# Kernel tuning notes

Hardware: AMD Instinct MI355X
Metric: run time of the kernel (lower is better)

## Reference

```python
import jax, jax.numpy as jnp
import numpy as np

# Dimensions pinned by the module: RelPosEmb1DAISummer(tokens=50, dim_head=124)
H = 8          # num_heads
D = 31         # channels // num_heads
T = 4          # time axis of the (p, t) spatial grid; D*T == 124 == dim_head
P = 50         # tokens
C = H * D      # 248 channels
SCALE = D ** -0.5  # note: module scales by d**-0.5 (=31), not (d*t)**-0.5 -- faithful


def rel_to_abs(x):
    """AI-Summer 1D relative->absolute reindexing. x: [b, h, l, 2l-1] -> [b, h, l, l]."""
    b, h, l, _ = x.shape
    x = jnp.pad(x, ((0, 0), (0, 0), (0, 0), (0, 1)))          # [b,h,l,2l]
    x = x.reshape(b, h, l * 2 * l)
    x = jnp.pad(x, ((0, 0), (0, 0), (0, l - 1)))
    x = x.reshape(b, h, l + 1, 2 * l - 1)
    return x[:, :, :l, l - 1:]


def setup_inputs() -> dict:
    key = jax.random.key(0)
    k1, k2, k3, k4 = jax.random.split(key, 4)
    B = 512
    x = jax.random.normal(k1, (B, C, P, T), jnp.float32)
    # 1x1 conv == per-position linear over channels: weight [3C, C], bias [3C]
    w_qkv = jax.random.normal(k2, (3 * C, C), jnp.float32) * (C ** -0.5)
    b_qkv = jax.random.normal(k3, (3 * C,), jnp.float32) * 0.01
    # shared-heads relative position embedding: [2*tokens-1, dim_head]
    rel_emb = jax.random.normal(k4, (2 * P - 1, D * T), jnp.float32) * ((D * T) ** -0.5)
    return {"x": x, "w_qkv": w_qkv, "b_qkv": b_qkv, "rel_emb": rel_emb}


def reference(x, w_qkv, b_qkv, rel_emb):
    B = x.shape[0]
    # 1x1 Conv2d: [B, C, P, T] -> [B, 3C, P, T]
    qkv = jnp.einsum('bcpt,oc->bopt', x, w_qkv) + b_qkv[None, :, None, None]
    # 'b (qkv h d) p t -> qkv b h d p t'
    qkv = qkv.reshape(B, 3, H, D, P, T)
    q, k, v = qkv[:, 0], qkv[:, 1], qkv[:, 2]                 # each [B,H,D,P,T]
    q = q.transpose(0, 1, 3, 2, 4).reshape(B, H, P, D * T)    # 'b h d p t -> b h p (d t)'
    k = k.transpose(0, 1, 2, 4, 3).reshape(B, H, D * T, P)    # 'b h d p t -> b h (d t) p'
    v = v.transpose(0, 1, 3, 2, 4).reshape(B, H, P, D * T)
    dots = jnp.einsum('bhpi,bhiq->bhpq', q, k)                # [B,H,P,P]
    bias = rel_to_abs(jnp.einsum('bhpd,rd->bhpr', q, rel_emb))
    attn = jax.nn.softmax((dots + bias) * SCALE, axis=-1)     # dropout = identity (eval)
    out = jnp.einsum('bhpq,bhqi->bhpi', attn, v)              # [B,H,P,D*T]
    # 'b h p (d t) -> b (h d) p t'
    out = out.reshape(B, H, P, D, T).transpose(0, 1, 3, 2, 4).reshape(B, H * D, P, T)
    return out
```

## Files before the change

### kernel.cpp

```cpp
#include <hip/hip_runtime.h>
#include <hip/hip_bf16.h>

typedef __bf16 bf16_t;
typedef bf16_t bf16x8 __attribute__((ext_vector_type(8)));
typedef bf16_t bf16x4 __attribute__((ext_vector_type(4)));
typedef float f32x4 __attribute__((ext_vector_type(4)));

constexpr float SCALE = 0.17960530202677491f;

__device__ __forceinline__ f32x4 mfma16(bf16x8 a, bf16x8 b, f32x4 c) {
    return __builtin_amdgcn_mfma_f32_16x16x32_bf16(a, b, c, 0, 0, 0);
}

__device__ __forceinline__ void opaque(bf16x8& v) {
    asm volatile("" : "+v"(v));
}

__global__ void prep_kernel(const float* __restrict__ w, const float* __restrict__ b_qkv,
                            const float* __restrict__ rel,
                            bf16_t* __restrict__ Wf, bf16_t* __restrict__ relf,
                            float* __restrict__ bp)
{
    int i = blockIdx.x * 256 + threadIdx.x;
    if (i < 196608) {
        int e = i & 7, lane = (i >> 3) & 63;
        int f = i >> 9;
        int ks = f & 7, g = f >> 3;
        int h = g / 6, m = g - h * 6;
        int r15 = lane & 15, g4 = lane >> 4;
        int s = m >> 1, d = ((m & 1) << 4) + r15;
        int c = ks * 32 + g4 * 8 + e;
        float v = 0.f;
        if (d < 31 && c < 248) v = w[(long)(s * 248 + h * 31 + d) * 248 + c];
        Wf[i] = (bf16_t)v;
        return;
    }
    i -= 196608;
    if (i < 14336) {
        int e = i & 7, lane = (i >> 3) & 63;
        int f = i >> 9;
        int ks = f & 3, rt = f >> 2;
        int r = rt * 16 + (lane & 15);
        int dt = ks * 32 + (lane >> 4) * 8 + e;
        float v = 0.f;
        if (r < 99 && dt < 124) v = rel[r * 124 + dt];
        relf[i] = (bf16_t)v;
        return;
    }
    i -= 14336;
    if (i < 768) {
        int h = i / 96, row = i - h * 96;
        int s = row >> 5, d = row & 31;
        bp[i] = (d < 31) ? b_qkv[s * 248 + h * 31 + d] : 0.f;
    }
}

__global__ void __launch_bounds__(512, 4)
fused_kernel(const float* __restrict__ x, const bf16_t* __restrict__ Wf,
             const bf16_t* __restrict__ relf, const float* __restrict__ bp,
             float* __restrict__ out)
{
    __shared__ __align__(16) bf16_t QH[64][128];
    __shared__ __align__(16) bf16_t KH[64][128];
    __shared__ __align__(16) bf16_t AS[64][64];
    __shared__ __align__(16) bf16_t VT[128][64];
    __shared__ float LS[50][68];

    const int b    = blockIdx.x;
    const int tid  = threadIdx.x;
    const int lane = tid & 63;
    const int w    = tid >> 6;
    const int r15  = lane & 15, g4 = lane >> 4;

    {
        *(f32x4*)((char*)&VT[0][0] + tid * 32)      = f32x4{0.f, 0.f, 0.f, 0.f};
        *(f32x4*)((char*)&VT[0][0] + tid * 32 + 16) = f32x4{0.f, 0.f, 0.f, 0.f};
        if (tid < 128) {
            int row = tid & 63;
            char* base = (tid < 64) ? (char*)&QH[0][0] : (char*)&KH[0][0];
            int chunk = 15 ^ (row & 7);
            *(long*)(base + row * 256 + chunk * 16 + 8) = 0L;
        }
    }

    const float* xb = x + (long)b * 49600;
    const int tile0 = w, tile1 = w + 8;
    const bool t1ok = (tile1 * 16 < 200);
    bf16x8 Areg[2][8];
#pragma unroll
    for (int ui = 0; ui < 2; ++ui) {
        int n = (w + 8 * ui) * 16 + r15;
        const float* xn = xb + n;
        bool nok = (n < 200);
#pragma unroll
        for (int ks = 0; ks < 8; ++ks) {
            bf16x8 fr;
#pragma unroll
            for (int e = 0; e < 8; ++e) {
                int c = ks * 32 + g4 * 8 + e;
                float v = (nok && c < 248) ? xn[(long)c * 200] : 0.f;
                fr[e] = (bf16_t)v;
            }
            Areg[ui][ks] = fr;
        }
    }
#pragma unroll
    for (int ui = 0; ui < 2; ++ui)
#pragma unroll
        for (int ks = 0; ks < 8; ++ks)
            opaque(Areg[ui][ks]);
    __syncthreads();

    const int qt  = w >> 1, par = w & 1;
    for (int h = 0; h < 8; ++h) {
        const bf16_t* wf = Wf + ((long)(h * 48) << 9) + lane * 8;
#pragma unroll
        for (int m = 0; m < 6; ++m) {
            f32x4 acc0 = f32x4{0.f, 0.f, 0.f, 0.f};
            f32x4 acc1 = f32x4{0.f, 0.f, 0.f, 0.f};
#pragma unroll
            for (int half = 0; half < 2; ++half) {
                bf16x8 Bc[4];
#pragma unroll
                for (int k4 = 0; k4 < 4; ++k4)
                    Bc[k4] = *(const bf16x8*)(wf + ((m * 8 + half * 4 + k4) << 9));
#pragma unroll
                for (int k4 = 0; k4 < 4; ++k4) {
                    int ks = half * 4 + k4;
                    acc0 = mfma16(Areg[0][ks], Bc[k4], acc0);
                    if (t1ok) acc1 = mfma16(Areg[1][ks], Bc[k4], acc1);
                }
            }
            int s = m >> 1;
            int d = ((m & 1) << 4) + r15;
            float bias = bp[h * 96 + m * 16 + r15];
            if (d < 31) {
#pragma unroll
                for (int ui = 0; ui < 2; ++ui) {
                    if (ui == 1 && !t1ok) continue;
                    f32x4 a = ui ? acc1 : acc0;
                    int p = (w + 8 * ui) * 4 + g4;
                    if (p >= 50) continue;
                    float a0 = a[0] + bias, a1 = a[1] + bias;
                    float a2 = a[2] + bias, a3 = a[3] + bias;
                    if (s < 2) {
                        bf16x4 pk = {(bf16_t)a0, (bf16_t)a1, (bf16_t)a2, (bf16_t)a3};
                        char* base = (s == 0) ? (char*)&QH[0][0] : (char*)&KH[0][0];
                        int chunk = (d >> 1) ^ (p & 7);
                        *(bf16x4*)(base + p * 256 + chunk * 16 + ((d & 1) << 3)) = pk;
                    } else {
                        int chunk = ((p >> 3) ^ (d & 7)) << 4;
                        char* vbase = (char*)&VT[0][0] + (d * 4) * 128 + chunk + (p & 7) * 2;
                        *(bf16_t*)(vbase)       = (bf16_t)a0;
                        *(bf16_t*)(vbase + 128) = (bf16_t)a1;
                        *(bf16_t*)(vbase + 256) = (bf16_t)a2;
                        *(bf16_t*)(vbase + 384) = (bf16_t)a3;
                    }
                }
            }
        }
        __syncthreads();

        bf16x8 Afr[4];
        {
            int p = qt * 16 + r15;
            int hp = p & 7;
#pragma unroll
            for (int ks = 0; ks < 4; ++ks)
                Afr[ks] = *(const bf16x8*)((char*)&QH[0][0] + p * 256 + ((((ks << 2) | g4) ^ hp) << 4));
        }
#pragma unroll
        for (int i = 0; i < 2; ++i) {
            int ct = par * 2 + i;
            int c = ct * 16 + r15;
            int hc = c & 7;
            f32x4 s = f32x4{0.f, 0.f, 0.f, 0.f};
#pragma unroll
            for (int ks = 0; ks < 4; ++ks) {
                bf16x8 Bf = *(const bf16x8*)((char*)&KH[0][0] + c * 256 + ((((ks << 2) | g4) ^ hc) << 4));
                s = mfma16(Afr[ks], Bf, s);
            }
            if (c < 50) {
#pragma unroll
                for (int j = 0; j < 4; ++j) {
                    int qrow = qt * 16 + g4 * 4 + j;
                    if (qrow < 50) LS[qrow][c] = s[j];
                }
            }
        }
        __syncthreads();

        {
            const bf16_t* rf = relf + lane * 8;
            for (int rt = par; rt < 7; rt += 2) {
                f32x4 s = f32x4{0.f, 0.f, 0.f, 0.f};
#pragma unroll
                for (int ks = 0; ks < 4; ++ks) {
                    bf16x8 R = *(const bf16x8*)(rf + ((rt * 4 + ks) << 9));
                    s = mfma16(Afr[ks], R, s);
                }
                int r = rt * 16 + r15;
#pragma unroll
                for (int j = 0; j < 4; ++j) {
                    int qrow = qt * 16 + g4 * 4 + j;
                    int jj = r + qrow - 49;
                    if (qrow < 50 && jj >= 0 && jj < 50) LS[qrow][jj] += s[j];
                }
            }
        }
        __syncthreads();

        {
            int row = tid >> 3, sub = tid & 7;
            int hrow = row & 7;
            if (row < 50) {
                float mx = -1e30f;
                for (int jj = sub; jj < 50; jj += 8) mx = fmaxf(mx, LS[row][jj]);
                mx = fmaxf(mx, __shfl_xor(mx, 1));
                mx = fmaxf(mx, __shfl_xor(mx, 2));
                mx = fmaxf(mx, __shfl_xor(mx, 4));
                float sum = 0.f;
                for (int jj = sub; jj < 50; jj += 8) {
                    float e = __expf((LS[row][jj] - mx) * SCALE);
                    LS[row][jj] = e;
                    sum += e;
                }
                sum += __shfl_xor(sum, 1);
                sum += __shfl_xor(sum, 2);
                sum += __shfl_xor(sum, 4);
                float rs = 1.f / sum;
                for (int jj = sub; jj < 64; jj += 8) {
                    float v = (jj < 50) ? LS[row][jj] * rs : 0.f;
                    *(bf16_t*)((char*)&AS[0][0] + row * 128 + (((jj >> 3) ^ hrow) << 4) + (jj & 7) * 2) = (bf16_t)v;
                }
            } else {
                for (int jj = sub; jj < 64; jj += 8)
                    *(bf16_t*)((char*)&AS[0][0] + row * 128 + (((jj >> 3) ^ hrow) << 4) + (jj & 7) * 2) = (bf16_t)0.f;
            }
        }
        __syncthreads();

        {
            int irow = w * 16 + r15;
            int hv = (irow >> 2) & 7;
            bf16x8 Av[2];
#pragma unroll
            for (int ks = 0; ks < 2; ++ks)
                Av[ks] = *(const bf16x8*)((char*)&VT[0][0] + irow * 128 + ((((ks << 2) | g4) ^ hv) << 4));
            int dd = w * 4 + g4;
#pragma unroll
            for (int pt = 0; pt < 4; ++pt) {
                int prow = pt * 16 + r15;
                int hp2 = prow & 7;
                f32x4 po = f32x4{0.f, 0.f, 0.f, 0.f};
#pragma unroll
                for (int ks = 0; ks < 2; ++ks) {
                    bf16x8 Bs = *(const bf16x8*)((char*)&AS[0][0] + prow * 128 + ((((ks << 2) | g4) ^ hp2) << 4));
                    po = mfma16(Av[ks], Bs, po);
                }
                if (dd < 31 && prow < 50)
                    *(f32x4*)(out + ((long)b * 248 + h * 31 + dd) * 200 + prow * 4) = po;
            }
        }
        __syncthreads();
    }
}

extern "C" void kernel_launch(void* const* d_in, const int* in_sizes, int n_in,
                              void* d_out, int out_size, void* d_ws, size_t ws_size,
                              hipStream_t stream)
{
    const float* x   = (const float*)d_in[0];
    const float* wq  = (const float*)d_in[1];
    const float* bq  = (const float*)d_in[2];
    const float* rel = (const float*)d_in[3];
    float* out = (float*)d_out;

    char* ws = (char*)d_ws;
    bf16_t* Wf   = (bf16_t*)ws;
    bf16_t* relf = (bf16_t*)(ws + 393216);
    float*  bp   = (float*)(ws + 421888);

    const int B = in_sizes[0] / 49600;

    prep_kernel<<<dim3(828), dim3(256), 0, stream>>>(wq, bq, rel, Wf, relf, bp);
    fused_kernel<<<dim3(B), dim3(512), 0, stream>>>(x, Wf, relf, bp, out);
}
```

Before: 205.4 us.

## Software-pipeline heads: split warps into score/softmax and PV groups with double buffers

Restructures the per-head loop into a two-stage pipeline. Warps 0-3 compute QK scores, the relative-position bias and the softmax for the current head. Warps 4-7 compute the attention-times-V output for the previous head, reading from double-buffered VT and AS regions carved out of one shared-memory array. This cuts the per-head barrier count from five to two, replacing intra-group barriers with lgkmcnt waits. It also prefetches weight and rel-embedding fragments one step ahead and folds SCALE into Q. The cost is more shared memory (about 80KB), which may lower occupancy, and an imbalanced split of work between the two warp groups.

New measurement: 346.2 us. +68.6%, slower.

```diff
diff --git a/kernel.cpp b/kernel.cpp
--- a/kernel.cpp
+++ b/kernel.cpp
@@ -8,10 +8,19 @@
 
 constexpr float SCALE = 0.17960530202677491f;
 
+#define QH_OFF 0
+#define KH_OFF 12800
+#define AS_OFF 25600
+#define VT_OFF 38400
+#define LS_OFF 70144
+#define SMEM_TOTAL 80544
+
 __device__ __forceinline__ f32x4 mfma16(bf16x8 a, bf16x8 b, f32x4 c) {
     return __builtin_amdgcn_mfma_f32_16x16x32_bf16(a, b, c, 0, 0, 0);
 }
-
+__device__ __forceinline__ void fence() {
+    asm volatile("s_waitcnt lgkmcnt(0)" ::: "memory");
+}
 __device__ __forceinline__ void opaque(bf16x8& v) {
     asm volatile("" : "+v"(v));
 }
@@ -60,12 +69,7 @@
              const bf16_t* __restrict__ relf, const float* __restrict__ bp,
              float* __restrict__ out)
 {
-    __shared__ __align__(16) bf16_t QH[64][128];
-    __shared__ __align__(16) bf16_t KH[64][128];
-    __shared__ __align__(16) bf16_t AS[64][64];
-    __shared__ __align__(16) bf16_t VT[128][64];
-    __shared__ float LS[50][68];
-
+    __shared__ __align__(16) char smem[SMEM_TOTAL];
     const int b    = blockIdx.x;
     const int tid  = threadIdx.x;
     const int lane = tid & 63;
@@ -73,19 +77,22 @@
     const int r15  = lane & 15, g4 = lane >> 4;
 
     {
-        *(f32x4*)((char*)&VT[0][0] + tid * 32)      = f32x4{0.f, 0.f, 0.f, 0.f};
-        *(f32x4*)((char*)&VT[0][0] + tid * 32 + 16) = f32x4{0.f, 0.f, 0.f, 0.f};
-        if (tid < 128) {
-            int row = tid & 63;
-            char* base = (tid < 64) ? (char*)&QH[0][0] : (char*)&KH[0][0];
+        f32x4 z = f32x4{0.f, 0.f, 0.f, 0.f};
+#pragma unroll
+        for (int k4 = 0; k4 < 4; ++k4) {
+            int idx = tid + k4 * 512;
+            if (idx < 1984) *(f32x4*)(smem + VT_OFF + idx * 16) = z;
+        }
+        if (tid < 100) {
+            int row = tid >> 1;
+            char* base = smem + ((tid & 1) ? KH_OFF : QH_OFF);
             int chunk = 15 ^ (row & 7);
             *(long*)(base + row * 256 + chunk * 16 + 8) = 0L;
         }
     }
 
     const float* xb = x + (long)b * 49600;
-    const int tile0 = w, tile1 = w + 8;
-    const bool t1ok = (tile1 * 16 < 200);
+    const bool t1ok = (w + 8) <= 12;
     bf16x8 Areg[2][8];
 #pragma unroll
     for (int ui = 0; ui < 2; ++ui) {
@@ -111,155 +118,189 @@
             opaque(Areg[ui][ks]);
     __syncthreads();
 
-    const int qt  = w >> 1, par = w & 1;
-    for (int h = 0; h < 8; ++h) {
-        const bf16_t* wf = Wf + ((long)(h * 48) << 9) + lane * 8;
-#pragma unroll
-        for (int m = 0; m < 6; ++m) {
-            f32x4 acc0 = f32x4{0.f, 0.f, 0.f, 0.f};
-            f32x4 acc1 = f32x4{0.f, 0.f, 0.f, 0.f};
-#pragma unroll
-            for (int half = 0; half < 2; ++half) {
-                bf16x8 Bc[4];
+    for (int it = 0; it <= 8; ++it) {
+        const int cur = it & 1, prv = cur ^ 1;
+
+        if (it < 8) {
+            const bf16_t* wf = Wf + ((long)(it * 48) << 9) + lane * 8;
+            char* VTc = smem + VT_OFF + cur * 15872;
+            bf16x8 B0[4];
+#pragma unroll
+            for (int k4 = 0; k4 < 4; ++k4)
+                B0[k4] = *(const bf16x8*)(wf + (k4 << 9));
+#pragma unroll
+            for (int m = 0; m < 6; ++m) {
+                bf16x8 B1[4];
 #pragma unroll
                 for (int k4 = 0; k4 < 4; ++k4)
-                    Bc[k4] = *(const bf16x8*)(wf + ((m * 8 + half * 4 + k4) << 9));
+                    B1[k4] = *(const bf16x8*)(wf + ((m * 8 + 4 + k4) << 9));
+                f32x4 acc0 = f32x4{0.f, 0.f, 0.f, 0.f};
+                f32x4 acc1 = f32x4{0.f, 0.f, 0.f, 0.f};
 #pragma unroll
                 for (int k4 = 0; k4 < 4; ++k4) {
-                    int ks = half * 4 + k4;
-                    acc0 = mfma16(Areg[0][ks], Bc[k4], acc0);
-                    if (t1ok) acc1 = mfma16(Areg[1][ks], Bc[k4], acc1);
+                    acc0 = mfma16(Areg[0][k4], B0[k4], acc0);
+                    if (t1ok) acc1 = mfma16(Areg[1][k4], B0[k4], acc1);
+                }
+                if (m < 5) {
+#pragma unroll
+                    for (int k4 = 0; k4 < 4; ++k4)
+                        B0[k4] = *(const bf16x8*)(wf + (((m + 1) * 8 + k4) << 9));
+                }
+#pragma unroll
+                for (int k4 = 0; k4 < 4; ++k4) {
+                    acc0 = mfma16(Areg[0][4 + k4], B1[k4], acc0);
+                    if (t1ok) acc1 = mfma16(Areg[1][4 + k4], B1[k4], acc1);
+                }
+                int s = m >> 1;
+                int d = ((m & 1) << 4) + r15;
+                float bias = bp[it * 96 + m * 16 + r15];
+                if (d < 31) {
+#pragma unroll
+                    for (int ui = 0; ui < 2; ++ui) {
+                        if (ui == 1 && !t1ok) continue;
+                        f32x4 a = ui ? acc1 : acc0;
+                        int p = (w + 8 * ui) * 4 + g4;
+                        if (p >= 50) continue;
+                        float a0 = a[0] + bias, a1 = a[1] + bias;
+                        float a2 = a[2] + bias, a3 = a[3] + bias;
+                        if (s == 0) { a0 *= SCALE; a1 *= SCALE; a2 *= SCALE; a3 *= SCALE; }
+                        if (s < 2) {
+                            bf16x4 pk = {(bf16_t)a0, (bf16_t)a1, (bf16_t)a2, (bf16_t)a3};
+                            char* base = smem + (s == 0 ? QH_OFF : KH_OFF);
+                            int chunk = (d >> 1) ^ (p & 7);
+                            *(bf16x4*)(base + p * 256 + chunk * 16 + ((d & 1) << 3)) = pk;
+                        } else {
+                            int chunkb = ((p >> 3) ^ (d & 7)) << 4;
+                            char* vb = VTc + (d * 4) * 128 + chunkb + (p & 7) * 2;
+                            *(bf16_t*)(vb)       = (bf16_t)a0;
+                            *(bf16_t*)(vb + 128) = (bf16_t)a1;
+                            *(bf16_t*)(vb + 256) = (bf16_t)a2;
+                            *(bf16_t*)(vb + 384) = (bf16_t)a3;
+                        }
+                    }
                 }
             }
-            int s = m >> 1;
-            int d = ((m & 1) << 4) + r15;
-            float bias = bp[h * 96 + m * 16 + r15];
-            if (d < 31) {
-#pragma unroll
-                for (int ui = 0; ui < 2; ++ui) {
-                    if (ui == 1 && !t1ok) continue;
-                    f32x4 a = ui ? acc1 : acc0;
-                    int p = (w + 8 * ui) * 4 + g4;
-                    if (p >= 50) continue;
-                    float a0 = a[0] + bias, a1 = a[1] + bias;
-                    float a2 = a[2] + bias, a3 = a[3] + bias;
-                    if (s < 2) {
-                        bf16x4 pk = {(bf16_t)a0, (bf16_t)a1, (bf16_t)a2, (bf16_t)a3};
-                        char* base = (s == 0) ? (char*)&QH[0][0] : (char*)&KH[0][0];
-                        int chunk = (d >> 1) ^ (p & 7);
-                        *(bf16x4*)(base + p * 256 + chunk * 16 + ((d & 1) << 3)) = pk;
-                    } else {
-                        int chunk = ((p >> 3) ^ (d & 7)) << 4;
-                        char* vbase = (char*)&VT[0][0] + (d * 4) * 128 + chunk + (p & 7) * 2;
-                        *(bf16_t*)(vbase)       = (bf16_t)a0;
-                        *(bf16_t*)(vbase + 128) = (bf16_t)a1;
-                        *(bf16_t*)(vbase + 256) = (bf16_t)a2;
-                        *(bf16_t*)(vbase + 384) = (bf16_t)a3;
+        }
+        __syncthreads();
+
+        if (w < 4) {
+            if (it < 8) {
+                const int qt = w;
+                bf16x8 Afr[4];
+                {
+                    int p = qt * 16 + r15;
+                    int hp = p & 7;
+#pragma unroll
+                    for (int ks = 0; ks < 4; ++ks)
+                        Afr[ks] = *(const bf16x8*)(smem + QH_OFF + p * 256 + ((((ks << 2) | g4) ^ hp) << 4));
+                }
+#pragma unroll
+                for (int ct = 0; ct < 4; ++ct) {
+                    int c = ct * 16 + r15;
+                    int hc = c & 7;
+                    f32x4 sA = f32x4{0.f, 0.f, 0.f, 0.f};
+#pragma unroll
+                    for (int ks = 0; ks < 4; ++ks) {
+                        bf16x8 Bf = *(const bf16x8*)(smem + KH_OFF + c * 256 + ((((ks << 2) | g4) ^ hc) << 4));
+                        sA = mfma16(Afr[ks], Bf, sA);
+                    }
+                    if (c < 50) {
+#pragma unroll
+                        for (int j = 0; j < 4; ++j) {
+                            int qrow = qt * 16 + g4 * 4 + j;
+                            if (qrow < 50)
+                                *(float*)(smem + LS_OFF + (qrow * 52 + c) * 4) = sA[j];
+                        }
+                    }
+                }
+                fence();
+                {
+                    const bf16_t* rf = relf + lane * 8;
+                    bf16x8 R0[4];
+#pragma unroll
+                    for (int ks = 0; ks < 4; ++ks) R0[ks] = *(const bf16x8*)(rf + (ks << 9));
+                    for (int rt = 0; rt < 7; ++rt) {
+                        bf16x8 R1[4];
+                        if (rt < 6) {
+#pragma unroll
+                            for (int ks = 0; ks < 4; ++ks)
+                                R1[ks] = *(const bf16x8*)(rf + (((rt + 1) * 4 + ks) << 9));
+                        }
+                        f32x4 sA = f32x4{0.f, 0.f, 0.f, 0.f};
+#pragma unroll
+                        for (int ks = 0; ks < 4; ++ks) sA = mfma16(Afr[ks], R0[ks], sA);
+                        int r = rt * 16 + r15;
+#pragma unroll
+                        for (int j = 0; j < 4; ++j) {
+                            int qrow = qt * 16 + g4 * 4 + j;
+                            int jj = r + qrow - 49;
+                            if (qrow < 50 && jj >= 0 && jj < 50)
+                                *(float*)(smem + LS_OFF + (qrow * 52 + jj) * 4) += sA[j];
+                        }
+#pragma unroll
+                        for (int ks = 0; ks < 4; ++ks) R0[ks] = R1[ks];
+                    }
+                }
+                fence();
+                {
+                    int row = qt * 16 + (lane >> 2);
+                    int quad = lane & 3;
+                    char* ASc = smem + AS_OFF + cur * 6400;
+                    if (row < 50) {
+                        float mx = -1e30f;
+                        for (int jj = quad; jj < 50; jj += 4)
+                            mx = fmaxf(mx, *(const float*)(smem + LS_OFF + (row * 52 + jj) * 4));
+                        mx = fmaxf(mx, __shfl_xor(mx, 1));
+                        mx = fmaxf(mx, __shfl_xor(mx, 2));
+                        float sum = 0.f;
+                        for (int jj = quad; jj < 50; jj += 4) {
+                            float* pL = (float*)(smem + LS_OFF + (row * 52 + jj) * 4);
+                            float e = __expf(*pL - mx);
+                            *pL = e;
+                            sum += e;
+                        }
+                        sum += __shfl_xor(sum, 1);
+                        sum += __shfl_xor(sum, 2);
+                        float rs = 1.f / sum;
+                        int hrow = row & 7;
+                        for (int jj = quad; jj < 64; jj += 4) {
+                            float v = (jj < 50)
+                                ? *(const float*)(smem + LS_OFF + (row * 52 + jj) * 4) * rs : 0.f;
+                            *(bf16_t*)(ASc + row * 128 + (((jj >> 3) ^ hrow) << 4) + (jj & 7) * 2) = (bf16_t)v;
+                        }
                     }
                 }
             }
-        }
-        __syncthreads();
-
-        bf16x8 Afr[4];
-        {
-            int p = qt * 16 + r15;
-            int hp = p & 7;
-#pragma unroll
-            for (int ks = 0; ks < 4; ++ks)
-                Afr[ks] = *(const bf16x8*)((char*)&QH[0][0] + p * 256 + ((((ks << 2) | g4) ^ hp) << 4));
-        }
-#pragma unroll
-        for (int i = 0; i < 2; ++i) {
-            int ct = par * 2 + i;
-            int c = ct * 16 + r15;
-            int hc = c & 7;
-            f32x4 s = f32x4{0.f, 0.f, 0.f, 0.f};
-#pragma unroll
-            for (int ks = 0; ks < 4; ++ks) {
-                bf16x8 Bf = *(const bf16x8*)((char*)&KH[0][0] + c * 256 + ((((ks << 2) | g4) ^ hc) << 4));
-                s = mfma16(Afr[ks], Bf, s);
-            }
-            if (c < 50) {
-#pragma unroll
-                for (int j = 0; j < 4; ++j) {
-                    int qrow = qt * 16 + g4 * 4 + j;
-                    if (qrow < 50) LS[qrow][c] = s[j];
-                }
-            }
-        }
-        __syncthreads();
-
-        {
-            const bf16_t* rf = relf + lane * 8;
-            for (int rt = par; rt < 7; rt += 2) {
-                f32x4 s = f32x4{0.f, 0.f, 0.f, 0.f};
-#pragma unroll
-                for (int ks = 0; ks < 4; ++ks) {
-                    bf16x8 R = *(const bf16x8*)(rf + ((rt * 4 + ks) << 9));
-                    s = mfma16(Afr[ks], R, s);
-                }
-                int r = rt * 16 + r15;
-#pragma unroll
-                for (int j = 0; j < 4; ++j) {
-                    int qrow = qt * 16 + g4 * 4 + j;
-                    int jj = r + qrow - 49;
-                    if (qrow < 50 && jj >= 0 && jj < 50) LS[qrow][jj] += s[j];
-                }
-            }
-        }
-        __syncthreads();
-
-        {
-            int row = tid >> 3, sub = tid & 7;
-            int hrow = row & 7;
-            if (row < 50) {
-                float mx = -1e30f;
-                for (int jj = sub; jj < 50; jj += 8) mx = fmaxf(mx, LS[row][jj]);
-                mx = fmaxf(mx, __shfl_xor(mx, 1));
-                mx = fmaxf(mx, __shfl_xor(mx, 2));
-                mx = fmaxf(mx, __shfl_xor(mx, 4));
-                float sum = 0.f;
-                for (int jj = sub; jj < 50; jj += 8) {
-                    float e = __expf((LS[row][jj] - mx) * SCALE);
-                    LS[row][jj] = e;
-                    sum += e;
-                }
-                sum += __shfl_xor(sum, 1);
-                sum += __shfl_xor(sum, 2);
-                sum += __shfl_xor(sum, 4);
-                float rs = 1.f / sum;
-                for (int jj = sub; jj < 64; jj += 8) {
-                    float v = (jj < 50) ? LS[row][jj] * rs : 0.f;
-                    *(bf16_t*)((char*)&AS[0][0] + row * 128 + (((jj >> 3) ^ hrow) << 4) + (jj & 7) * 2) = (bf16_t)v;
-                }
-            } else {
-                for (int jj = sub; jj < 64; jj += 8)
-                    *(bf16_t*)((char*)&AS[0][0] + row * 128 + (((jj >> 3) ^ hrow) << 4) + (jj & 7) * 2) = (bf16_t)0.f;
-            }
-        }
-        __syncthreads();
-
-        {
-            int irow = w * 16 + r15;
-            int hv = (irow >> 2) & 7;
-            bf16x8 Av[2];
-#pragma unroll
-            for (int ks = 0; ks < 2; ++ks)
-                Av[ks] = *(const bf16x8*)((char*)&VT[0][0] + irow * 128 + ((((ks << 2) | g4) ^ hv) << 4));
-            int dd = w * 4 + g4;
-#pragma unroll
-            for (int pt = 0; pt < 4; ++pt) {
-                int prow = pt * 16 + r15;
-                int hp2 = prow & 7;
-                f32x4 po = f32x4{0.f, 0.f, 0.f, 0.f};
-#pragma unroll
-                for (int ks = 0; ks < 2; ++ks) {
-                    bf16x8 Bs = *(const bf16x8*)((char*)&AS[0][0] + prow * 128 + ((((ks << 2) | g4) ^ hp2) << 4));
-                    po = mfma16(Av[ks], Bs, po);
-                }
-                if (dd < 31 && prow < 50)
-                    *(f32x4*)(out + ((long)b * 248 + h * 31 + dd) * 200 + prow * 4) = po;
+        } else {
+            if (it > 0) {
+                const int hh = it - 1;
+                const int wv = w - 4;
+                const char* VTp = smem + VT_OFF + prv * 15872;
+                const char* ASp = smem + AS_OFF + prv * 6400;
+#pragma unroll
+                for (int ii = 0; ii < 2; ++ii) {
+                    int itile = wv * 2 + ii;
+                    int irow = itile * 16 + r15;
+                    int hv = (irow >> 2) & 7;
+                    bf16x8 Av[2];
+#pragma unroll
+                    for (int ks = 0; ks < 2; ++ks)
+                        Av[ks] = *(const bf16x8*)(VTp + irow * 128 + ((((ks << 2) | g4) ^ hv) << 4));
+                    int dd = itile * 4 + g4;
+#pragma unroll
+                    for (int pt = 0; pt < 4; ++pt) {
+                        int prow = pt * 16 + r15;
+                        int hp2 = prow & 7;
+                        f32x4 po = f32x4{0.f, 0.f, 0.f, 0.f};
+#pragma unroll
+                        for (int ks = 0; ks < 2; ++ks) {
+                            bf16x8 Bs = *(const bf16x8*)(ASp + prow * 128 + ((((ks << 2) | g4) ^ hp2) << 4));
+                            po = mfma16(Av[ks], Bs, po);
+                        }
+                        if (dd < 31 && prow < 50)
+                            *(f32x4*)(out + ((long)b * 248 + hh * 31 + dd) * 200 + prow * 4) = po;
+                    }
+                }
             }
         }
         __syncthreads();
```
